# Kernel tuning notes

Measured on AMD Instinct MI355X. Metric: run time of the kernel, lower is better.

## Reference

```python
import jax, jax.numpy as jnp
import numpy as np

D_MODEL = 1024
N_HEADS = 16
D_KV = 64
INNER = N_HEADS * D_KV  # 1024


def setup_inputs() -> dict:
    key = jax.random.key(0)
    ks = jax.random.split(key, 6)
    B, SV, ST = 4, 1024, 1024
    vis = jax.random.normal(ks[0], (B, SV, D_MODEL), dtype=jnp.float32)
    txt = jax.random.normal(ks[1], (B, ST, D_MODEL), dtype=jnp.float32)
    s = 0.02
    Wq = jax.random.normal(ks[2], (D_MODEL, INNER), dtype=jnp.float32) * s
    Wk = jax.random.normal(ks[3], (D_MODEL, INNER), dtype=jnp.float32) * s
    Wv = jax.random.normal(ks[4], (D_MODEL, INNER), dtype=jnp.float32) * s
    Wo = jax.random.normal(ks[5], (INNER, D_MODEL), dtype=jnp.float32) * s
    return {"vis_hidden_states": vis, "txt_hidden_states": txt,
            "Wq": Wq, "Wk": Wk, "Wv": Wv, "Wo": Wo}


def _split_heads(x):
    # [B, S, INNER] -> [B, H, S, Dk]
    B, S, _ = x.shape
    return x.reshape(B, S, N_HEADS, D_KV).transpose(0, 2, 1, 3)


def _merge_heads(x):
    # [B, H, S, Dk] -> [B, S, INNER]
    B, H, S, Dk = x.shape
    return x.transpose(0, 2, 1, 3).reshape(B, S, H * Dk)


def reference(vis_hidden_states, txt_hidden_states, Wq, Wk, Wv, Wo):
    # T5-style attention: NO 1/sqrt(d) scaling, no biases.
    q = _split_heads(vis_hidden_states @ Wq)   # [B,H,Sv,Dk]
    k = _split_heads(txt_hidden_states @ Wk)   # [B,H,St,Dk]
    v = _split_heads(txt_hidden_states @ Wv)   # [B,H,St,Dk]
    v2 = _split_heads(vis_hidden_states @ Wv)  # [B,H,Sv,Dk]

    scores = jnp.einsum('bhqd,bhkd->bhqk', q, k)  # [B,H,Sv,St]
    attn = jax.nn.softmax(scores.astype(jnp.float32), axis=-1).astype(scores.dtype)

    vis_out = jnp.einsum('bhqk,bhkd->bhqd', attn, v)   # softmax-normalized over k
    txt_out = jnp.einsum('bhqk,bhqd->bhkd', attn, v2)  # transposed attn, NOT renormalized

    vis_out = _merge_heads(vis_out) @ Wo  # [B,Sv,D]
    txt_out = _merge_heads(txt_out) @ Wo  # [B,St,D]
    return vis_out, txt_out
```

## Files before the change

kernel.cpp:

```cpp
#include <hip/hip_runtime.h>

typedef unsigned short u16;
typedef unsigned int u32;
typedef __bf16 bf16x8 __attribute__((ext_vector_type(8)));
typedef float f32x4 __attribute__((ext_vector_type(4)));
typedef u16 u16x4 __attribute__((ext_vector_type(4)));
typedef __attribute__((address_space(1))) void* as1_t;
typedef __attribute__((address_space(3))) void* as3_t;

#define LOG2E 1.4426950408889634f
#define MFMA(a,b,c) __builtin_amdgcn_mfma_f32_16x16x32_bf16(a,b,c,0,0,0)

__device__ __forceinline__ u16 f2bf(float f){
  u32 u = __float_as_uint(f);
  return (u16)((u + 0x7FFFu + ((u >> 16) & 1u)) >> 16);
}
__device__ __forceinline__ float bf2f(u16 x){
  return __uint_as_float(((u32)x) << 16);
}
#if __has_builtin(__builtin_amdgcn_cvt_pk_bf16_f32)
__device__ __forceinline__ u16x4 pk4(float a, float b, float c, float d){
  auto lo = __builtin_amdgcn_cvt_pk_bf16_f32(a,b);
  auto hi = __builtin_amdgcn_cvt_pk_bf16_f32(c,d);
  union { u16x4 v; u32 w[2]; } u;
  u.w[0] = __builtin_bit_cast(u32, lo);
  u.w[1] = __builtin_bit_cast(u32, hi);
  return u.v;
}
#else
__device__ __forceinline__ u16x4 pk4(float a, float b, float c, float d){
  u16x4 r = { f2bf(a), f2bf(b), f2bf(c), f2bf(d) };
  return r;
}
#endif
__device__ __forceinline__ void gld16(const u16* gp, u16* lp){
  __builtin_amdgcn_global_load_lds((as1_t)(u16*)gp, (as3_t)lp, 16, 0, 0);
}

#define SBAR  __builtin_amdgcn_s_barrier()
#define SCHB  __builtin_amdgcn_sched_barrier(0)
#define SP1   __builtin_amdgcn_s_setprio(1)
#define SP0   __builtin_amdgcn_s_setprio(0)
#define WAITL0 asm volatile("s_waitcnt lgkmcnt(0)" ::: "memory")
#define WAITV6 asm volatile("s_waitcnt vmcnt(6)" ::: "memory")
#define WV2 asm volatile("s_waitcnt vmcnt(2)" ::: "memory")
#define WV8 asm volatile("s_waitcnt vmcnt(8)" ::: "memory")

__global__ void prep_kernel(const float* __restrict__ vis, u16* __restrict__ vis16,
                            const float* __restrict__ txt, u16* __restrict__ txt16,
                            const float* __restrict__ Wq, const float* __restrict__ Wk,
                            const float* __restrict__ Wv, const float* __restrict__ Wo,
                            u16* __restrict__ T0, u16* __restrict__ T1,
                            u16* __restrict__ T2, u16* __restrict__ T3,
                            u16* __restrict__ T4){
  int bid = blockIdx.x;
  if(bid < 8192){
    const float* src = (bid < 4096) ? vis : txt;
    u16* dst = (bid < 4096) ? vis16 : txt16;
    int idx = ((bid & 4095)*256 + threadIdx.x)*4;
    float4 v = *(const float4*)(src + idx);
    *(u16x4*)(dst + idx) = pk4(v.x, v.y, v.z, v.w);
    return;
  }
  int rr = bid - 8192;
  int wi = rr >> 8, tile = rr & 255;
  const float* W; u16* WT;
  switch(wi){
    case 0: W = Wq; WT = T0; break;
    case 1: W = Wv; WT = T1; break;
    case 2: W = Wk; WT = T2; break;
    case 3: W = Wv; WT = T3; break;
    default: W = Wo; WT = T4; break;
  }
  __shared__ u16 t[64][65];
  int bn = (tile & 15)*64, bk = (tile >> 4)*64;
  int c = threadIdx.x & 63, r0 = threadIdx.x >> 6;
  #pragma unroll
  for(int j=0;j<64;j+=4){
    int r = r0 + j;
    t[r][c] = f2bf(W[(bk + r)*1024 + bn + c]);
  }
  __syncthreads();
  #pragma unroll
  for(int j=0;j<64;j+=4){
    int r = r0 + j;
    WT[(bn + r)*1024 + bk + c] = t[c][r];
  }
}

#define STG(G, gbase, dsto, kk) { \
    _Pragma("unroll") \
    for(int ii=0;ii<4;ii++){ \
      int slot_ = ii*512 + tid; int r_ = slot_ >> 3, cs_ = slot_ & 7; \
      gld16((G) + (size_t)((gbase) + r_)*1024 + (kk) + ((cs_ ^ (r_ & 7)) << 3), \
            lds + (dsto) + (ii*512 + (w << 6))*8); } }

#define LDA_(bo, mh) { \
    _Pragma("unroll") \
    for(int q_=0;q_<4;q_++){ \
      int ro_ = (bo) + arow + (((mh)*4 + q_) << 10); \
      af[q_][0] = *(const bf16x8*)(lds + ro_ + sx0); \
      af[q_][1] = *(const bf16x8*)(lds + ro_ + sx1); } }

#define LDB_(bo, nh, bfv) { \
    _Pragma("unroll") \
    for(int j_=0;j_<2;j_++){ \
      int ro_ = (bo) + brow + (((nh)*2 + j_) << 10); \
      bfv[j_][0] = *(const bf16x8*)(lds + ro_ + sx0); \
      bfv[j_][1] = *(const bf16x8*)(lds + ro_ + sx1); } }

#define MM_N(mh, bfv, nh) { \
    _Pragma("unroll") \
    for(int q_=0;q_<4;q_++) \
      _Pragma("unroll") \
      for(int j_=0;j_<2;j_++){ \
        int ai_ = ((mh)*4+q_)*4 + (nh)*2+j_; \
        acc[ai_] = MFMA(af[q_][0], bfv[j_][0], acc[ai_]); \
        acc[ai_] = MFMA(af[q_][1], bfv[j_][1], acc[ai_]); } }

#define MM_T(mh, bfv, nh) { \
    _Pragma("unroll") \
    for(int q_=0;q_<4;q_++) \
      _Pragma("unroll") \
      for(int j_=0;j_<2;j_++){ \
        int ai_ = ((nh)*2+j_)*8 + (mh)*4+q_; \
        acc[ai_] = MFMA(bfv[j_][0], af[q_][0], acc[ai_]); \
        acc[ai_] = MFMA(bfv[j_][1], af[q_][1], acc[ai_]); } }

#define TILE_BODY(bufo, ts, MM) { \
    LDA_(bufo, 0); LDB_(bufo, 0, bfv0); \
    SBAR; WAITL0; SCHB; SP1; MM(0, bfv0, 0); SP0; SBAR; \
    LDB_(bufo, 1, bfv1); \
    SBAR; WAITL0; SCHB; SP1; MM(0, bfv1, 1); SP0; SBAR; \
    LDA_(bufo, 1); \
    SBAR; WAITL0; SCHB; SP1; MM(1, bfv1, 1); SP0; SBAR; \
    STG(A , bm, (bufo)        , ts); \
    STG(Bt, bn, (bufo) + 16384, ts); \
    SCHB; SP1; MM(1, bfv0, 0); SP0; \
    WV8; SBAR; }

__global__ __launch_bounds__(512, 2)
void proj_gemm_kernel(const u16* __restrict__ Avis, const u16* __restrict__ Atxt,
                      const u16* __restrict__ Wvis, const u16* __restrict__ Wtxt,
                      u16* __restrict__ Qb, u16* __restrict__ V2t,
                      u16* __restrict__ Kb, u16* __restrict__ Vt)
{
  const u16 *A, *Bt; u16 *Cn, *Ct;
  if(blockIdx.z == 0){ A = Avis; Bt = Wvis; Cn = Qb; Ct = V2t; }
  else               { A = Atxt; Bt = Wtxt; Cn = Kb; Ct = Vt;  }
  __shared__ u16 lds[65536];
  const int tid = threadIdx.x, w = tid >> 6, lane = tid & 63;
  const int quad = lane >> 4, cl = lane & 15;
  const int wr = w >> 2, wc = w & 3;
  const int bm = blockIdx.x*256, bn = blockIdx.y*256;
  const int sx0 = ((quad    ) ^ (cl & 7)) << 3;
  const int sx1 = ((quad + 4) ^ (cl & 7)) << 3;
  const int arow = ((wr << 7) + cl) << 6;
  const int brow = (((wc << 6) + cl) << 6) + 16384;

  f32x4 acc[32];
  #pragma unroll
  for(int a=0;a<32;a++){ f32x4 z = {0.f,0.f,0.f,0.f}; acc[a] = z; }
  bf16x8 af[4][2], bfv0[2][2], bfv1[2][2];

  STG(A , bm, 0,     0);  STG(Bt, bn, 16384, 0);
  STG(A , bm, 32768, 64); STG(Bt, bn, 32768+16384, 64);
  WV8; SBAR;

  if(bn < 1024){
    for(int tt=0; tt<8; tt++){
      const int t0 = 2*tt;
      TILE_BODY(0,     ((t0+2)&15) << 6, MM_N);
      TILE_BODY(32768, ((t0+3)&15) << 6, MM_N);
    }
    #pragma unroll
    for(int mf=0; mf<8; mf++){
      int m0 = bm + wr*128 + mf*16 + quad*4;
      #pragma unroll
      for(int nf=0; nf<4; nf++){
        int n = bn + wc*64 + nf*16 + cl;
        int h = n >> 6, d = n & 63;
        #pragma unroll
        for(int i2=0;i2<4;i2++){
          int m = m0 + i2; int b = m >> 10, s = m & 1023;
          Cn[(((size_t)(b*16 + h)*1024 + s) << 6) + d] = f2bf(acc[mf*4+nf][i2]);
        }
      }
    }
  } else {
    for(int tt=0; tt<8; tt++){
      const int t0 = 2*tt;
      TILE_BODY(0,     ((t0+2)&15) << 6, MM_T);
      TILE_BODY(32768, ((t0+3)&15) << 6, MM_T);
    }
    const int bT = bm >> 10;
    const int sbase = (bm & 1023) + wr*128;
    #pragma unroll
    for(int nf=0; nf<4; nf++){
      #pragma unroll
      for(int i2=0;i2<4;i2++){
        int nn = (bn - 1024) + wc*64 + nf*16 + quad*4 + i2;
        int h = nn >> 6, d = nn & 63;
        u16* rowp = Ct + ((size_t)(bT*16 + h)*64 + d)*1024;
        #pragma unroll
        for(int mf=0; mf<8; mf++)
          rowp[sbase + mf*16 + cl] = f2bf(acc[nf*8+mf][i2]);
      }
    }
  }
}

#undef STG
#undef LDA_
#undef LDB_
#undef MM_N
#undef MM_T
#undef TILE_BODY

__device__ __forceinline__ void gemm_pipe(const u16* __restrict__ A,
                                          const u16* __restrict__ Bt,
                                          int bm, int bn,
                                          u16* __restrict__ lds,
                                          f32x4 (&acc)[4][4],
                                          int tid, int w, int quad, int cl,
                                          int wr, int wc)
{
  const int sx0 = ((quad    ) ^ (cl & 7)) << 3;
  const int sx1 = ((quad + 4) ^ (cl & 7)) << 3;
  const int arow = ((wr << 6) + cl) << 6;
  const int brow = (((wc << 6) + cl) << 6) + 16384;
  bf16x8 af[4][2], bfv[2][2];

#define STAGE128(G, gbase, dsto, kk) { \
    _Pragma("unroll") \
    for(int ii=0;ii<2;ii++){ \
      int slot_ = ii*512 + tid; int r_ = slot_ >> 3, cs_ = slot_ & 7; \
      gld16((G) + (size_t)((gbase) + r_)*1024 + (kk) + ((cs_ ^ (r_ & 7)) << 3), \
            lds + (dsto) + (ii*512 + (w << 6))*8); } }

#define LDA_(bo) { \
    _Pragma("unroll") \
    for(int m_=0;m_<4;m_++){ \
      int ro_ = (bo) + arow + (m_ << 10); \
      af[m_][0] = *(const bf16x8*)(lds + ro_ + sx0); \
      af[m_][1] = *(const bf16x8*)(lds + ro_ + sx1); } }

#define LDB_(bo, nh) { \
    _Pragma("unroll") \
    for(int j_=0;j_<2;j_++){ \
      int ro_ = (bo) + brow + (((nh)*2 + j_) << 10); \
      bfv[j_][0] = *(const bf16x8*)(lds + ro_ + sx0); \
      bfv[j_][1] = *(const bf16x8*)(lds + ro_ + sx1); } }

#define MM_(nh) { \
    _Pragma("unroll") \
    for(int m_=0;m_<4;m_++) \
      _Pragma("unroll") \
      for(int j_=0;j_<2;j_++){ \
        acc[m_][(nh)*2+j_] = MFMA(af[m_][0], bfv[j_][0], acc[m_][(nh)*2+j_]); \
        acc[m_][(nh)*2+j_] = MFMA(af[m_][1], bfv[j_][1], acc[m_][(nh)*2+j_]); } }

  STAGE128(A , bm      , 0,          0);
  STAGE128(A , bm + 128, 8192,       0);
  STAGE128(Bt, bn      , 16384,      0);
  STAGE128(A , bm      , 24576,      64);
  STAGE128(A , bm + 128, 24576+8192, 64);
  STAGE128(Bt, bn      , 24576+16384,64);
  WAITV6; SBAR;

  #pragma unroll 2
  for(int t=0;t<16;t++){
    const int c  = (t % 3) * 24576;
    const int n2 = ((t+2) % 3) * 24576;
    const int ts = ((t+2) & 15) << 6;
    LDA_(c); LDB_(c, 0);
    STAGE128(A, bm      , n2,        ts);
    STAGE128(A, bm + 128, n2 + 8192, ts);
    SBAR; WAITL0; SCHB;
    SP1; MM_(0); SP0;
    SBAR;
    LDB_(c, 1);
    STAGE128(Bt, bn, n2 + 16384, ts);
    SBAR; WAITL0; SCHB;
    SP1; MM_(1); SP0;
    WAITV6;
    SBAR;
  }
#undef STAGE128
#undef LDA_
#undef LDB_
#undef MM_
}

__global__ __launch_bounds__(512, 2)
void out_gemm_kernel(const u16* __restrict__ A, const u16* __restrict__ Bt,
                     float* __restrict__ Cf)
{
  __shared__ u16 lds[73728];
  const int tid = threadIdx.x, w = tid >> 6, lane = tid & 63;
  const int quad = lane >> 4, cl = lane & 15;
  const int wr = w >> 1, wc = w & 1;
  const int bm = blockIdx.x*256, bn = blockIdx.y*128;

  f32x4 acc[4][4];
  #pragma unroll
  for(int a=0;a<4;a++)
    #pragma unroll
    for(int b=0;b<4;b++){ f32x4 z = {0.f,0.f,0.f,0.f}; acc[a][b] = z; }

  gemm_pipe(A, Bt, bm, bn, lds, acc, tid, w, quad, cl, wr, wc);

  #pragma unroll
  for(int mf=0; mf<4; mf++)
    #pragma unroll
    for(int nf=0; nf<4; nf++)
      #pragma unroll
      for(int i=0;i<4;i++){
        int m = bm + wr*64 + mf*16 + quad*4 + i;
        int n = bn + wc*64 + nf*16 + cl;
        Cf[(size_t)m*1024 + n] = acc[mf][nf][i];
      }
}

__global__ __launch_bounds__(512, 4)
void attn_vis_kernel(const u16* __restrict__ Q, const u16* __restrict__ Kc,
                     const u16* __restrict__ Vt, u16* __restrict__ visA,
                     float* __restrict__ rl_g)
{
  __shared__ u16 lds[25600];
  u16* Pl  = lds;
  const int tid = threadIdx.x, w = tid>>6, lane = tid&63;
  const int quad = lane>>4, cl = lane&15;
  const int bh = blockIdx.x, q0 = blockIdx.y*128;
  const u16* Qh  = Q  + (size_t)bh*65536;
  const u16* Kh  = Kc + (size_t)bh*65536;
  const u16* Vth = Vt + (size_t)bh*65536;

  #pragma unroll
  for(int i=0;i<2;i++){
    int slot = i*512 + tid;
    int c = slot >> 7, r = slot & 127;
    gld16(Qh + (size_t)(q0 + r)*64 + c*8, Pl + slot*8);
  }
  __syncthreads();
  bf16x8 qf[2];
  #pragma unroll
  for(int kk=0;kk<2;kk++)
    qf[kk] = *(const bf16x8*)(Pl + ((kk*4+quad)*128 + w*16 + cl)*8);
  __syncthreads();

#define KVST(kt, buf) { \
    u16* B_ = lds + 9216 + (buf)*8192; \
    { int c_ = tid >> 6, r_ = tid & 63; \
      gld16(Kh + (size_t)((kt)*64 + r_)*64 + c_*8, B_ + tid*8); } \
    { int d_ = tid >> 3, ch_ = tid & 7; \
      gld16(Vth + (size_t)d_*1024 + (kt)*64 + ((ch_^(d_&7))*8), B_ + 4096 + tid*8); } }

  KVST(0, 0); KVST(1, 1);
  WV2; SBAR;

  float lrun = 0.f;
  f32x4 oacc[4];
  #pragma unroll
  for(int dt=0;dt<4;dt++){ f32x4 z = {0.f,0.f,0.f,0.f}; oacc[dt] = z; }

  for(int kt=0;kt<16;kt++){
    const int bb = kt & 1;
    u16* Kst = lds + 9216 + bb*8192;
    u16* Vst = Kst + 4096;
    #pragma unroll
    for(int mtk=0;mtk<4;mtk++){
      f32x4 s = {0.f,0.f,0.f,0.f};
      #pragma unroll
      for(int kk=0;kk<2;kk++){
        bf16x8 ka = *(const bf16x8*)(Kst + ((kk*4+quad)*64 + mtk*16 + cl)*8);
        s = MFMA(ka, qf[kk], s);
      }
      float p0 = __builtin_amdgcn_exp2f(s[0]*LOG2E);
      float p1 = __builtin_amdgcn_exp2f(s[1]*LOG2E);
      float p2 = __builtin_amdgcn_exp2f(s[2]*LOG2E);
      float p3 = __builtin_amdgcn_exp2f(s[3]*LOG2E);
      lrun += (p0+p1)+(p2+p3);
      *(u16x4*)(Pl + (w*16 + cl)*72 + mtk*16 + quad*4) = pk4(p0,p1,p2,p3);
    }
    bf16x8 pa[2];
    #pragma unroll
    for(int kk=0;kk<2;kk++)
      pa[kk] = *(const bf16x8*)(Pl + (w*16 + cl)*72 + kk*32 + quad*8);
    #pragma unroll
    for(int dt=0;dt<4;dt++){
      int d = dt*16 + cl;
      #pragma unroll
      for(int kk=0;kk<2;kk++){
        bf16x8 vb = *(const bf16x8*)(Vst + d*64 + (((kk*4+quad)^(d&7))*8));
        oacc[dt] = MFMA(pa[kk], vb, oacc[dt]);
      }
    }
    SBAR;
    const int nk = (kt < 14) ? kt + 2 : kt;
    KVST(nk, bb);
    WV2;
    SBAR;
  }
#undef KVST
  lrun += __shfl_xor(lrun, 16, 64);
  lrun += __shfl_xor(lrun, 32, 64);
  float rl = 1.f/lrun;
  if(quad == 0) rl_g[bh*1024 + q0 + w*16 + cl] = rl;
  const int b = bh >> 4, h = bh & 15;
  #pragma unroll
  for(int i=0;i<4;i++){
    float rr = __shfl(rl, quad*4 + i, 16);
    int q = q0 + w*16 + quad*4 + i;
    #pragma unroll
    for(int dt=0;dt<4;dt++)
      visA[(size_t)(b*1024 + q)*1024 + h*64 + dt*16 + cl] = f2bf(oacc[dt][i]*rr);
  }
}

__global__ __launch_bounds__(512, 4)
void attn_txt_kernel(const u16* __restrict__ Kc, const u16* __restrict__ Q,
                     const u16* __restrict__ V2t, const float* __restrict__ rl_g,
                     u16* __restrict__ txtA)
{
  __shared__ u16 lds[27648];
  u16* Pl  = lds;
  u16* rlL = lds + 25600;
  const float* rlF = (const float*)rlL;
  const int tid = threadIdx.x, w = tid>>6, lane = tid&63;
  const int quad = lane>>4, cl = lane&15;
  const int bh = blockIdx.x, k0 = blockIdx.y*128;
  const u16* Kh  = Kc  + (size_t)bh*65536;
  const u16* Qh  = Q   + (size_t)bh*65536;
  const u16* Vth = V2t + (size_t)bh*65536;

  #pragma unroll
  for(int i=0;i<2;i++){
    int slot = i*512 + tid;
    int c = slot >> 7, r = slot & 127;
    gld16(Kh + (size_t)(k0 + r)*64 + c*8, Pl + slot*8);
  }
  if(tid < 256)
    gld16((const u16*)(rl_g + (size_t)bh*1024) + tid*8, rlL + tid*8);
  __syncthreads();
  bf16x8 kb[2];
  #pragma unroll
  for(int kk=0;kk<2;kk++)
    kb[kk] = *(const bf16x8*)(Pl + ((kk*4+quad)*128 + w*16 + cl)*8);
  __syncthreads();

#define QVST(qt, buf) { \
    u16* B_ = lds + 9216 + (buf)*8192; \
    { int c_ = tid >> 6, r_ = tid & 63; \
      gld16(Qh + (size_t)((qt)*64 + r_)*64 + c_*8, B_ + tid*8); } \
    { int d_ = tid >> 3, ch_ = tid & 7; \
      gld16(Vth + (size_t)d_*1024 + (qt)*64 + ((ch_^(d_&7))*8), B_ + 4096 + tid*8); } }

  QVST(0, 0); QVST(1, 1);
  WV2; SBAR;

  f32x4 oacc[4];
  #pragma unroll
  for(int dt=0;dt<4;dt++){ f32x4 z = {0.f,0.f,0.f,0.f}; oacc[dt] = z; }

  for(int qt=0;qt<16;qt++){
    const int bb = qt & 1;
    u16* Qst = lds + 9216 + bb*8192;
    u16* Vst = Qst + 4096;
    f32x4 rv[4];
    #pragma unroll
    for(int mtq=0;mtq<4;mtq++)
      rv[mtq] = *(const f32x4*)(rlF + qt*64 + mtq*16 + quad*4);
    #pragma unroll
    for(int mtq=0;mtq<4;mtq++){
      f32x4 s = {0.f,0.f,0.f,0.f};
      #pragma unroll
      for(int kk=0;kk<2;kk++){
        bf16x8 qa = *(const bf16x8*)(Qst + ((kk*4+quad)*64 + mtq*16 + cl)*8);
        s = MFMA(qa, kb[kk], s);
      }
      float p0 = __builtin_amdgcn_exp2f(s[0]*LOG2E)*rv[mtq][0];
      float p1 = __builtin_amdgcn_exp2f(s[1]*LOG2E)*rv[mtq][1];
      float p2 = __builtin_amdgcn_exp2f(s[2]*LOG2E)*rv[mtq][2];
      float p3 = __builtin_amdgcn_exp2f(s[3]*LOG2E)*rv[mtq][3];
      *(u16x4*)(Pl + (w*16 + cl)*72 + mtq*16 + quad*4) = pk4(p0,p1,p2,p3);
    }
    bf16x8 pa[2];
    #pragma unroll
    for(int kk=0;kk<2;kk++)
      pa[kk] = *(const bf16x8*)(Pl + (w*16 + cl)*72 + kk*32 + quad*8);
    #pragma unroll
    for(int dt=0;dt<4;dt++){
      int d = dt*16 + cl;
      #pragma unroll
      for(int kk=0;kk<2;kk++){
        bf16x8 vb = *(const bf16x8*)(Vst + d*64 + (((kk*4+quad)^(d&7))*8));
        oacc[dt] = MFMA(pa[kk], vb, oacc[dt]);
      }
    }
    SBAR;
    const int nq = (qt < 14) ? qt + 2 : qt;
    QVST(nq, bb);
    WV2;
    SBAR;
  }
#undef QVST
  const int b = bh >> 4, h = bh & 15;
  #pragma unroll
  for(int i=0;i<4;i++){
    int k = k0 + w*16 + quad*4 + i;
    #pragma unroll
    for(int dt=0;dt<4;dt++)
      txtA[(size_t)(b*1024 + k)*1024 + h*64 + dt*16 + cl] = f2bf(oacc[dt][i]);
  }
}

extern "C" void kernel_launch(void* const* d_in, const int* in_sizes, int n_in,
                              void* d_out, int out_size, void* d_ws, size_t ws_size,
                              hipStream_t stream)
{
  const float* vis = (const float*)d_in[0];
  const float* txt = (const float*)d_in[1];
  const float* Wq  = (const float*)d_in[2];
  const float* Wk  = (const float*)d_in[3];
  const float* Wv  = (const float*)d_in[4];
  const float* Wo  = (const float*)d_in[5];
  float* out = (float*)d_out;

  char* ws = (char*)d_ws;
  const size_t MB = 1u << 20;
  u16* vis16 = (u16*)(ws + 0);
  u16* txt16 = (u16*)(ws + 8*MB);
  u16* Wvis  = (u16*)(ws + 16*MB);
  u16* Wtxt  = (u16*)(ws + 20*MB);
  u16* Qb    = (u16*)(ws + 24*MB);
  u16* Kb    = (u16*)(ws + 32*MB);
  u16* Vt    = (u16*)(ws + 40*MB);
  u16* V2t   = (u16*)(ws + 48*MB);
  float* rl_g = (float*)(ws + 56*MB);
  u16* WoT   = (u16*)(ws + 57*MB);
  u16* visA = vis16;  u16* txtA = txt16;

  prep_kernel<<<9472, 256, 0, stream>>>(vis, vis16, txt, txt16,
                                        Wq, Wk, Wv, Wo,
                                        Wvis, Wvis + 1048576, Wtxt, Wtxt + 1048576, WoT);
  proj_gemm_kernel<<<dim3(16,8,2), 512, 0, stream>>>(vis16, txt16, Wvis, Wtxt,
                                                     Qb, V2t, Kb, Vt);
  attn_vis_kernel<<<dim3(64,8), 512, 0, stream>>>(Qb, Kb, Vt, visA, rl_g);
  attn_txt_kernel<<<dim3(64,8), 512, 0, stream>>>(Kb, Qb, V2t, rl_g, txtA);
  out_gemm_kernel<<<dim3(32,8), 512, 0, stream>>>(visA, WoT, out);
}
```

Measured before the change: 214.9 us.

## Shrink output GEMM tiles to 128x128 with simple double-buffered pipeline

Replaces the 256x128, 512-thread, triple-buffered output projection GEMM with a 128x128 tile kernel using 256 threads and a double-buffered LDS loop synchronized by __syncthreads each K step. The grid doubles to 512 blocks, which aims at better CU occupancy and load balance, and LDS use drops per block. In exchange, data reuse per tile falls and the finer-grained barrier/priority interleaving that overlapped loads with MFMA is removed. With a full barrier each iteration, global loads may be waited on more conservatively.

```diff
diff --git a/kernel.cpp b/kernel.cpp
--- a/kernel.cpp
+++ b/kernel.cpp
@@ -42,7 +42,6 @@
 #define SP1   __builtin_amdgcn_s_setprio(1)
 #define SP0   __builtin_amdgcn_s_setprio(0)
 #define WAITL0 asm volatile("s_waitcnt lgkmcnt(0)" ::: "memory")
-#define WAITV6 asm volatile("s_waitcnt vmcnt(6)" ::: "memory")
 #define WV2 asm volatile("s_waitcnt vmcnt(2)" ::: "memory")
 #define WV8 asm volatile("s_waitcnt vmcnt(8)" ::: "memory")
 
@@ -217,98 +216,69 @@
 #undef MM_T
 #undef TILE_BODY
 
-__device__ __forceinline__ void gemm_pipe(const u16* __restrict__ A,
-                                          const u16* __restrict__ Bt,
-                                          int bm, int bn,
-                                          u16* __restrict__ lds,
-                                          f32x4 (&acc)[4][4],
-                                          int tid, int w, int quad, int cl,
-                                          int wr, int wc)
+#define STGO(G, gbase, dsto, kk) { \
+    _Pragma("unroll") \
+    for(int ii=0;ii<4;ii++){ \
+      int slot_ = ii*256 + tid; int r_ = slot_ >> 3, cs_ = slot_ & 7; \
+      gld16((G) + (size_t)((gbase) + r_)*1024 + (kk) + ((cs_ ^ (r_ & 7)) << 3), \
+            lds + (dsto) + (ii*256 + (w << 6))*8); } }
+
+__global__ __launch_bounds__(256, 2)
+void out_gemm_kernel(const u16* __restrict__ A, const u16* __restrict__ Bt,
+                     float* __restrict__ Cf)
 {
+  __shared__ u16 lds[32768];
+  const int tid = threadIdx.x, w = tid >> 6, lane = tid & 63;
+  const int quad = lane >> 4, cl = lane & 15;
+  const int wr = w >> 1, wc = w & 1;
+  const int bm = blockIdx.x*128, bn = blockIdx.y*128;
   const int sx0 = ((quad    ) ^ (cl & 7)) << 3;
   const int sx1 = ((quad + 4) ^ (cl & 7)) << 3;
   const int arow = ((wr << 6) + cl) << 6;
-  const int brow = (((wc << 6) + cl) << 6) + 16384;
-  bf16x8 af[4][2], bfv[2][2];
-
-#define STAGE128(G, gbase, dsto, kk) { \
-    _Pragma("unroll") \
-    for(int ii=0;ii<2;ii++){ \
-      int slot_ = ii*512 + tid; int r_ = slot_ >> 3, cs_ = slot_ & 7; \
-      gld16((G) + (size_t)((gbase) + r_)*1024 + (kk) + ((cs_ ^ (r_ & 7)) << 3), \
-            lds + (dsto) + (ii*512 + (w << 6))*8); } }
-
-#define LDA_(bo) { \
-    _Pragma("unroll") \
-    for(int m_=0;m_<4;m_++){ \
-      int ro_ = (bo) + arow + (m_ << 10); \
-      af[m_][0] = *(const bf16x8*)(lds + ro_ + sx0); \
-      af[m_][1] = *(const bf16x8*)(lds + ro_ + sx1); } }
-
-#define LDB_(bo, nh) { \
-    _Pragma("unroll") \
-    for(int j_=0;j_<2;j_++){ \
-      int ro_ = (bo) + brow + (((nh)*2 + j_) << 10); \
-      bfv[j_][0] = *(const bf16x8*)(lds + ro_ + sx0); \
-      bfv[j_][1] = *(const bf16x8*)(lds + ro_ + sx1); } }
-
-#define MM_(nh) { \
-    _Pragma("unroll") \
-    for(int m_=0;m_<4;m_++) \
-      _Pragma("unroll") \
-      for(int j_=0;j_<2;j_++){ \
-        acc[m_][(nh)*2+j_] = MFMA(af[m_][0], bfv[j_][0], acc[m_][(nh)*2+j_]); \
-        acc[m_][(nh)*2+j_] = MFMA(af[m_][1], bfv[j_][1], acc[m_][(nh)*2+j_]); } }
-
-  STAGE128(A , bm      , 0,          0);
-  STAGE128(A , bm + 128, 8192,       0);
-  STAGE128(Bt, bn      , 16384,      0);
-  STAGE128(A , bm      , 24576,      64);
-  STAGE128(A , bm + 128, 24576+8192, 64);
-  STAGE128(Bt, bn      , 24576+16384,64);
-  WAITV6; SBAR;
+  const int brow = (((wc << 6) + cl) << 6) + 8192;
+
+  f32x4 acc[4][4];
+  #pragma unroll
+  for(int a=0;a<4;a++)
+    #pragma unroll
+    for(int b=0;b<4;b++){ f32x4 z = {0.f,0.f,0.f,0.f}; acc[a][b] = z; }
+  bf16x8 af[4][2], bfv[4][2];
+
+  STGO(A , bm, 0,    0);
+  STGO(Bt, bn, 8192, 0);
+  __syncthreads();
 
   #pragma unroll 2
-  for(int t=0;t<16;t++){
-    const int c  = (t % 3) * 24576;
-    const int n2 = ((t+2) % 3) * 24576;
-    const int ts = ((t+2) & 15) << 6;
-    LDA_(c); LDB_(c, 0);
-    STAGE128(A, bm      , n2,        ts);
-    STAGE128(A, bm + 128, n2 + 8192, ts);
-    SBAR; WAITL0; SCHB;
-    SP1; MM_(0); SP0;
-    SBAR;
-    LDB_(c, 1);
-    STAGE128(Bt, bn, n2 + 16384, ts);
-    SBAR; WAITL0; SCHB;
-    SP1; MM_(1); SP0;
-    WAITV6;
-    SBAR;
-  }
-#undef STAGE128
-#undef LDA_
-#undef LDB_
-#undef MM_
-}
-
-__global__ __launch_bounds__(512, 2)
-void out_gemm_kernel(const u16* __restrict__ A, const u16* __restrict__ Bt,
-                     float* __restrict__ Cf)
-{
-  __shared__ u16 lds[73728];
-  const int tid = threadIdx.x, w = tid >> 6, lane = tid & 63;
-  const int quad = lane >> 4, cl = lane & 15;
-  const int wr = w >> 1, wc = w & 1;
-  const int bm = blockIdx.x*256, bn = blockIdx.y*128;
-
-  f32x4 acc[4][4];
-  #pragma unroll
-  for(int a=0;a<4;a++)
-    #pragma unroll
-    for(int b=0;b<4;b++){ f32x4 z = {0.f,0.f,0.f,0.f}; acc[a][b] = z; }
-
-  gemm_pipe(A, Bt, bm, bn, lds, acc, tid, w, quad, cl, wr, wc);
+  for(int t=0; t<16; ++t){
+    const int c  = (t & 1) << 14;
+    const int nb = c ^ 16384;
+    if(t < 15){
+      STGO(A , bm, nb,        (t+1) << 6);
+      STGO(Bt, bn, nb + 8192, (t+1) << 6);
+    }
+    #pragma unroll
+    for(int m=0;m<4;m++){
+      int ro = c + arow + (m << 10);
+      af[m][0] = *(const bf16x8*)(lds + ro + sx0);
+      af[m][1] = *(const bf16x8*)(lds + ro + sx1);
+    }
+    #pragma unroll
+    for(int n=0;n<4;n++){
+      int ro = c + brow + (n << 10);
+      bfv[n][0] = *(const bf16x8*)(lds + ro + sx0);
+      bfv[n][1] = *(const bf16x8*)(lds + ro + sx1);
+    }
+    SP1;
+    #pragma unroll
+    for(int m=0;m<4;m++)
+      #pragma unroll
+      for(int n=0;n<4;n++){
+        acc[m][n] = MFMA(af[m][0], bfv[n][0], acc[m][n]);
+        acc[m][n] = MFMA(af[m][1], bfv[n][1], acc[m][n]);
+      }
+    SP0;
+    __syncthreads();
+  }
 
   #pragma unroll
   for(int mf=0; mf<4; mf++)
@@ -321,6 +291,7 @@
         Cf[(size_t)m*1024 + n] = acc[mf][nf][i];
       }
 }
+#undef STGO
 
 __global__ __launch_bounds__(512, 4)
 void attn_vis_kernel(const u16* __restrict__ Q, const u16* __restrict__ Kc,
@@ -548,5 +519,5 @@
                                                      Qb, V2t, Kb, Vt);
   attn_vis_kernel<<<dim3(64,8), 512, 0, stream>>>(Qb, Kb, Vt, visA, rl_g);
   attn_txt_kernel<<<dim3(64,8), 512, 0, stream>>>(Kb, Qb, V2t, rl_g, txtA);
-  out_gemm_kernel<<<dim3(32,8), 512, 0, stream>>>(visA, WoT, out);
-}
+  out_gemm_kernel<<<dim3(64,8), 256, 0, stream>>>(visA, WoT, out);
+}
```

Result: faster. 209.5 us (-2.5%).
